# Kernel optimization log

Measured on AMD Instinct MI355X. Metric: run time of the kernel, lower is better.

Reference implementation:

```python
import jax, jax.numpy as jnp
import numpy as np

B = 32768
F = 256
H1 = 16
H2 = 8

def setup_inputs() -> dict:
    key = jax.random.key(0)
    ks = jax.random.split(key, 9)
    x = jax.random.normal(ks[0], (B, F), dtype=jnp.float32)
    # Stacked per-feature MLP params (one UnivariateNetwork per feature)
    W1 = jax.random.normal(ks[1], (F, H1), dtype=jnp.float32) * (1.0 / np.sqrt(1))
    b1 = jax.random.normal(ks[2], (F, H1), dtype=jnp.float32) * 0.05
    W2 = jax.random.normal(ks[3], (F, H1, H2), dtype=jnp.float32) * (1.0 / np.sqrt(H1))
    b2 = jax.random.normal(ks[4], (F, H2), dtype=jnp.float32) * 0.05
    W3 = jax.random.normal(ks[5], (F, H2), dtype=jnp.float32) * (1.0 / np.sqrt(H2))
    b3 = jax.random.normal(ks[6], (F,), dtype=jnp.float32) * 0.05
    theta = jax.random.uniform(ks[7], (F,), dtype=jnp.float32) * 0.05
    bias = jnp.zeros((1,), dtype=jnp.float32)
    return {"x": x, "W1": W1, "b1": b1, "W2": W2, "b2": b2,
            "W3": W3, "b3": b3, "theta": theta, "bias": bias}

def reference(x, W1, b1, W2, b2, W3, b3, theta, bias):
    # Batched per-feature MLP: 1 -> H1 -> H2 -> 1 with ELU, all features at once.
    h1 = jax.nn.elu(x[:, :, None] * W1[None, :, :] + b1[None, :, :])      # [B, F, H1]
    h2 = jax.nn.elu(jnp.einsum('bfh,fhk->bfk', h1, W2) + b2[None, :, :])  # [B, F, H2]
    Z = jnp.einsum('bfk,fk->bf', h2, W3) + b3[None, :]                    # [B, F]
    weights = jax.nn.softplus(theta)                                      # [F]
    y_pred = Z @ weights + bias                                           # [B]
    return (y_pred, weights, Z)
```

## Files before the change

kernel.cpp:

```cpp
#include <hip/hip_runtime.h>

#define NB 32768
#define NF 256
#define H1 16
#define H2 8
#define ROWS_PER_BLOCK 1024
#define ITERS (ROWS_PER_BLOCK / 64)
#define FPB 4
#define NT (FPB * 64)

__device__ __forceinline__ float elu_f(float v) {
    return v > 0.0f ? v : (__expf(v) - 1.0f);
}
__device__ __forceinline__ float rfl(float v) {
    return __int_as_float(__builtin_amdgcn_readfirstlane(__float_as_int(v)));
}

__global__ __launch_bounds__(NT, 6)
void z_kernel(const float* __restrict__ x,  const float* __restrict__ W1,
              const float* __restrict__ b1, const float* __restrict__ W2,
              const float* __restrict__ b2, const float* __restrict__ W3,
              const float* __restrict__ b3, float* __restrict__ z_out) {
    const int wave = threadIdx.x >> 6;
    const int lane = threadIdx.x & 63;
    const int f    = blockIdx.y * FPB + wave;
    const int rowBase = blockIdx.x * ROWS_PER_BLOCK;

    __shared__ float lds_w2[FPB][64];

    if (lane < 16) {
        const float4 v = reinterpret_cast<const float4*>(W2 + f * H1 * H2 + 64)[lane];
        reinterpret_cast<float4*>(lds_w2[wave])[lane] = v;
    }

    float s_w2[8 * H2];
    {
        const float4* p = reinterpret_cast<const float4*>(W2 + f * H1 * H2);
        #pragma unroll
        for (int i = 0; i < 16; ++i) {
            float4 v = p[i];
            s_w2[4*i]   = rfl(v.x); s_w2[4*i+1] = rfl(v.y);
            s_w2[4*i+2] = rfl(v.z); s_w2[4*i+3] = rfl(v.w);
        }
    }
    float w1v[H1], s_b1[H1];
    {
        const float4* pw = reinterpret_cast<const float4*>(W1 + f * H1);
        const float4* pb = reinterpret_cast<const float4*>(b1 + f * H1);
        #pragma unroll
        for (int i = 0; i < 4; ++i) {
            float4 v = pw[i];
            w1v[4*i] = v.x; w1v[4*i+1] = v.y; w1v[4*i+2] = v.z; w1v[4*i+3] = v.w;
        }
        #pragma unroll
        for (int i = 0; i < 4; ++i) {
            float4 v = pb[i];
            s_b1[4*i]   = rfl(v.x); s_b1[4*i+1] = rfl(v.y);
            s_b1[4*i+2] = rfl(v.z); s_b1[4*i+3] = rfl(v.w);
        }
    }
    float b2v[H2];
    {
        const float4* p = reinterpret_cast<const float4*>(b2 + f * H2);
        float4 v0 = p[0], v1 = p[1];
        b2v[0]=v0.x; b2v[1]=v0.y; b2v[2]=v0.z; b2v[3]=v0.w;
        b2v[4]=v1.x; b2v[5]=v1.y; b2v[6]=v1.z; b2v[7]=v1.w;
    }
    float s_w3[H2];
    {
        const float4* p = reinterpret_cast<const float4*>(W3 + f * H2);
        float4 v0 = p[0], v1 = p[1];
        s_w3[0]=rfl(v0.x); s_w3[1]=rfl(v0.y); s_w3[2]=rfl(v0.z); s_w3[3]=rfl(v0.w);
        s_w3[4]=rfl(v1.x); s_w3[5]=rfl(v1.y); s_w3[6]=rfl(v1.z); s_w3[7]=rfl(v1.w);
    }
    const float s_b3 = rfl(b3[f]);

    __syncthreads();

    const float* wbase = lds_w2[wave];

    int off = (rowBase + lane) * NF + f;
    float xv = x[off];

    #pragma unroll 1
    for (int it = 0; it < ITERS; ++it) {
        const int noff = off + 64 * NF;
        const float xn = x[(it + 1 < ITERS) ? noff : off];

        float acc[H2];
        #pragma unroll
        for (int k = 0; k < H2; ++k) acc[k] = b2v[k];

        #pragma unroll
        for (int h = 0; h < 8; ++h) {
            const float h1 = elu_f(fmaf(xv, w1v[h], s_b1[h]));
            #pragma unroll
            for (int k = 0; k < H2; ++k)
                acc[k] = fmaf(h1, s_w2[h * H2 + k], acc[k]);
        }

        int dsoff = 0;
        asm volatile("" : "+v"(dsoff));
        const float4* wp = reinterpret_cast<const float4*>(wbase + dsoff);
        #pragma unroll
        for (int h = 0; h < 8; ++h) {
            const float4 wlo = wp[2 * h];
            const float4 whi = wp[2 * h + 1];
            const float h1 = elu_f(fmaf(xv, w1v[8 + h], s_b1[8 + h]));
            acc[0] = fmaf(h1, wlo.x, acc[0]);
            acc[1] = fmaf(h1, wlo.y, acc[1]);
            acc[2] = fmaf(h1, wlo.z, acc[2]);
            acc[3] = fmaf(h1, wlo.w, acc[3]);
            acc[4] = fmaf(h1, whi.x, acc[4]);
            acc[5] = fmaf(h1, whi.y, acc[5]);
            acc[6] = fmaf(h1, whi.z, acc[6]);
            acc[7] = fmaf(h1, whi.w, acc[7]);
        }

        float z = s_b3;
        #pragma unroll
        for (int k = 0; k < H2; ++k)
            z = fmaf(elu_f(acc[k]), s_w3[k], z);

        z_out[off] = z;
        off = noff; xv = xn;
    }
}

#define NT2 256
#define ROWS2 64
__global__ __launch_bounds__(NT2, 4)
void y_kernel(const float* __restrict__ z, const float* __restrict__ theta,
              const float* __restrict__ bias, float* __restrict__ y_out,
              float* __restrict__ w_out) {
    __shared__ __align__(16) float wls[NF];
    const int tid = threadIdx.x;
    {
        const float th = theta[tid];
        const float w  = logf(1.0f + __expf(th));
        wls[tid] = w;
        if (blockIdx.x == 0) w_out[tid] = w;
    }
    __syncthreads();
    const int wave = tid >> 6, lane = tid & 63;
    const float4 w4 = reinterpret_cast<const float4*>(wls)[lane];
    const float biasv = bias[0];
    #pragma unroll 1
    for (int r = 0; r < ROWS2 / 4; ++r) {
        const int row = blockIdx.x * ROWS2 + wave * (ROWS2 / 4) + r;
        const float4 zv = reinterpret_cast<const float4*>(z + row * NF)[lane];
        float s = zv.x * w4.x + zv.y * w4.y + zv.z * w4.z + zv.w * w4.w;
        #pragma unroll
        for (int o = 32; o > 0; o >>= 1) s += __shfl_down(s, o, 64);
        if (lane == 0) y_out[row] = s + biasv;
    }
}

extern "C" void kernel_launch(void* const* d_in, const int* in_sizes, int n_in,
                              void* d_out, int out_size, void* d_ws, size_t ws_size,
                              hipStream_t stream) {
    const float* x     = (const float*)d_in[0];
    const float* W1    = (const float*)d_in[1];
    const float* b1    = (const float*)d_in[2];
    const float* W2    = (const float*)d_in[3];
    const float* b2    = (const float*)d_in[4];
    const float* W3    = (const float*)d_in[5];
    const float* b3    = (const float*)d_in[6];
    const float* theta = (const float*)d_in[7];
    const float* bias  = (const float*)d_in[8];

    float* y_out = (float*)d_out;
    float* w_out = y_out + NB;
    float* z_out = w_out + NF;

    dim3 grid1(NB / ROWS_PER_BLOCK, NF / FPB);
    z_kernel<<<grid1, NT, 0, stream>>>(x, W1, b1, W2, b2, W3, b3, z_out);
    y_kernel<<<NB / ROWS2, NT2, 0, stream>>>(z_out, theta, bias, y_out, w_out);
}
```

Before: 167.3 us.

## Software-pipeline first-layer ELU computation one iteration ahead in z_kernel

Computes the first-layer activations for the next row chunk while doing the second-layer FMAs for the current chunk, and prefetches x two iterations ahead instead of one. The aim is to interleave the independent exp/ELU work with the FMA chain and hide global load latency. This costs 16 extra live registers, so the occupancy hint is lowered from 6 to 5 blocks per CU.

```diff
diff --git a/kernel.cpp b/kernel.cpp
--- a/kernel.cpp
+++ b/kernel.cpp
@@ -16,7 +16,7 @@
     return __int_as_float(__builtin_amdgcn_readfirstlane(__float_as_int(v)));
 }
 
-__global__ __launch_bounds__(NT, 6)
+__global__ __launch_bounds__(NT, 5)
 void z_kernel(const float* __restrict__ x,  const float* __restrict__ W1,
               const float* __restrict__ b1, const float* __restrict__ W2,
               const float* __restrict__ b2, const float* __restrict__ W3,
@@ -79,13 +79,21 @@
 
     const float* wbase = lds_w2[wave];
 
-    int off = (rowBase + lane) * NF + f;
-    float xv = x[off];
+    const int off0 = (rowBase + lane) * NF + f;
+    float h1c[H1];
+    {
+        const float xv = x[off0];
+        #pragma unroll
+        for (int h = 0; h < H1; ++h)
+            h1c[h] = elu_f(fmaf(xv, w1v[h], s_b1[h]));
+    }
+    float xn  = x[off0 + 64 * NF];
+    int off = off0;
 
     #pragma unroll 1
     for (int it = 0; it < ITERS; ++it) {
-        const int noff = off + 64 * NF;
-        const float xn = x[(it + 1 < ITERS) ? noff : off];
+        const int off2 = off + 2 * 64 * NF;
+        const float xnn = x[(it + 2 < ITERS) ? off2 : off];
 
         float acc[H2];
         #pragma unroll
@@ -93,10 +101,11 @@
 
         #pragma unroll
         for (int h = 0; h < 8; ++h) {
-            const float h1 = elu_f(fmaf(xv, w1v[h], s_b1[h]));
+            const float hc = h1c[h];
+            h1c[h] = elu_f(fmaf(xn, w1v[h], s_b1[h]));
             #pragma unroll
             for (int k = 0; k < H2; ++k)
-                acc[k] = fmaf(h1, s_w2[h * H2 + k], acc[k]);
+                acc[k] = fmaf(hc, s_w2[h * H2 + k], acc[k]);
         }
 
         int dsoff = 0;
@@ -106,15 +115,16 @@
         for (int h = 0; h < 8; ++h) {
             const float4 wlo = wp[2 * h];
             const float4 whi = wp[2 * h + 1];
-            const float h1 = elu_f(fmaf(xv, w1v[8 + h], s_b1[8 + h]));
-            acc[0] = fmaf(h1, wlo.x, acc[0]);
-            acc[1] = fmaf(h1, wlo.y, acc[1]);
-            acc[2] = fmaf(h1, wlo.z, acc[2]);
-            acc[3] = fmaf(h1, wlo.w, acc[3]);
-            acc[4] = fmaf(h1, whi.x, acc[4]);
-            acc[5] = fmaf(h1, whi.y, acc[5]);
-            acc[6] = fmaf(h1, whi.z, acc[6]);
-            acc[7] = fmaf(h1, whi.w, acc[7]);
+            const float hc = h1c[8 + h];
+            h1c[8 + h] = elu_f(fmaf(xn, w1v[8 + h], s_b1[8 + h]));
+            acc[0] = fmaf(hc, wlo.x, acc[0]);
+            acc[1] = fmaf(hc, wlo.y, acc[1]);
+            acc[2] = fmaf(hc, wlo.z, acc[2]);
+            acc[3] = fmaf(hc, wlo.w, acc[3]);
+            acc[4] = fmaf(hc, whi.x, acc[4]);
+            acc[5] = fmaf(hc, whi.y, acc[5]);
+            acc[6] = fmaf(hc, whi.z, acc[6]);
+            acc[7] = fmaf(hc, whi.w, acc[7]);
         }
 
         float z = s_b3;
@@ -123,7 +133,7 @@
             z = fmaf(elu_f(acc[k]), s_w3[k], z);
 
         z_out[off] = z;
-        off = noff; xv = xn;
+        off += 64 * NF; xn = xnn;
     }
 }
 
```

Result: faster. 162.4 us (-3.0%).
